# Performance work log

Hardware: AMD Instinct MI355X
Metric: run time of the kernel (lower is better)

## Reference

```python
import jax, jax.numpy as jnp
import numpy as np

B, N, C, F = 64, 64, 8, 256      # batch, neighbors per sample, in_channels, in_features
OC, OF = 8, 256                  # out_channels, out_features


def setup_inputs() -> dict:
    key = jax.random.key(0)
    k0, k1, k2, k3, k4 = jax.random.split(key, 5)
    x = jax.random.normal(k0, (B, C, F), dtype=jnp.float32)
    neighbor = jax.random.normal(k1, (B, N, C, F), dtype=jnp.float32)
    # att1/att2: nn.Linear(in_features, in_channels, bias=False) -> weight (C, F)
    W1 = jax.random.normal(k2, (C, F), dtype=jnp.float32) * (1.0 / np.sqrt(F))
    W2 = jax.random.normal(k3, (C, F), dtype=jnp.float32) * (1.0 / np.sqrt(F))
    # conv: nn.Conv1d(C, OC*OF, kernel_size=F, bias=False) -> weight (OC*OF, C, F)
    Wc = jax.random.normal(k4, (OC * OF, C, F), dtype=jnp.float32) * (1.0 / np.sqrt(C * F))
    return {"x": x, "neighbor": neighbor, "W1": W1, "W2": W2, "Wc": Wc}


def _sgnroot(a):
    return jnp.sign(a) * jnp.sqrt(jnp.clip(jnp.abs(a), 1e-8))


def _row_normalize(a):
    # torch: x / (x.abs().sum(1, keepdim=True) + 1e-7); dim 1 is the channel dim of (B,C,F,F)
    a = a / (jnp.abs(a).sum(axis=1, keepdims=True) + 1e-7)
    return jnp.where(jnp.isnan(a), 0.0, a)


def _feature_adjacency(x, neighbor, W1, W2):
    # w[b,n] = sum_{c,k} (x[b] @ W1^T)[c,k] * sum_{k,l} (neighbor[b,n] @ W2^T)[k,l]
    s1 = jnp.einsum('bcf,kf->b', x, W1)            # total sum of att1(x[b])
    s2 = jnp.einsum('bncf,kf->bn', neighbor, W2)   # total sum of att2(y[b,n])
    w = s1[:, None] * s2                            # (B, N)
    # fadj[b,c,a,d] = sum_n x[b,c,a] * neighbor[b,n,c,d] * w[b,n]
    fadj = jnp.einsum('bca,bncd,bn->bcad', x, neighbor, w)
    fadj = fadj + jnp.swapaxes(fadj, -2, -1)
    return _row_normalize(_sgnroot(fadj))


def _conv_transform(z, Wc, lead_shape):
    # Conv1d(C, OC*OF, kernel_size=F, bias=False) over (.., C, F) == full contraction
    out = jnp.einsum('...cf,ocf->...o', z, Wc)
    return out.reshape(*lead_shape, OC, OF)


def reference(x, neighbor, W1, W2, Wc):
    adj = _feature_adjacency(x, neighbor, W1, W2)              # (B,C,F,F)
    # transform(x, adj): (adj @ x.unsqueeze(-1)).squeeze(-1) then conv
    zx = jnp.einsum('bcad,bcd->bca', adj, x)                   # (B,C,F)
    x_out = _conv_transform(zx, Wc, (x.shape[0],))             # (B,OC,OF)
    # transform(neighbor[i], adj[i:i+1]) for each i -> adj broadcasts over N
    zn = jnp.einsum('bcad,bncd->bnca', adj, neighbor)          # (B,N,C,F)
    n_out = _conv_transform(zn, Wc, (x.shape[0], neighbor.shape[1]))  # (B,N,OC,OF)
    return x_out, n_out
```

## Files before the change

### kernel.cpp

```cpp
#include <hip/hip_runtime.h>
#include <hip/hip_bf16.h>
#include <math.h>

#define B_ 64
#define N_ 64
#define C_ 8
#define F_ 256
#define K_ 2048
#define NO_ 2048
#define M_TOT 4160

typedef __attribute__((ext_vector_type(8))) short bf16x8;
typedef __attribute__((ext_vector_type(4))) float f32x4;

__device__ __forceinline__ unsigned short bfbits(float f) {
    union { __hip_bfloat16 h; unsigned short u; } cv;
    cv.h = __float2bfloat16(f);
    return cv.u;
}

__global__ __launch_bounds__(256) void sums_wc_k(const float* __restrict__ x,
        const float* __restrict__ nb, const float* __restrict__ W1,
        const float* __restrict__ W2, const float* __restrict__ Wc,
        float* __restrict__ s1, float* __restrict__ s2,
        __hip_bfloat16* __restrict__ Bbuf) {
    int blk = blockIdx.x;
    int f = threadIdx.x;
    if (blk >= B_ * N_ + B_) {
        int i = (blk - (B_ * N_ + B_)) * 1024 + f * 4;
        float4 v = *(const float4*)(Wc + i);
        ushort4 u = { bfbits(v.x), bfbits(v.y), bfbits(v.z), bfbits(v.w) };
        *(ushort4*)(&Bbuf[i]) = u;
        return;
    }
    float val;
    if (blk < B_ * N_) {
        const float* base = nb + (size_t)blk * (C_ * F_);
        float wsum = 0.f;
        #pragma unroll
        for (int k = 0; k < C_; ++k) wsum += W2[k * F_ + f];
        float cs = 0.f;
        #pragma unroll
        for (int c = 0; c < C_; ++c) cs += base[c * F_ + f];
        val = cs * wsum;
    } else {
        int b = blk - B_ * N_;
        const float* base = x + (size_t)b * (C_ * F_);
        float wsum = 0.f;
        #pragma unroll
        for (int k = 0; k < C_; ++k) wsum += W1[k * F_ + f];
        float cs = 0.f;
        #pragma unroll
        for (int c = 0; c < C_; ++c) cs += base[c * F_ + f];
        val = cs * wsum;
    }
    #pragma unroll
    for (int off = 32; off > 0; off >>= 1) val += __shfl_down(val, off, 64);
    __shared__ float wred[4];
    int w = f >> 6;
    if ((f & 63) == 0) wred[w] = val;
    __syncthreads();
    if (f == 0) {
        float s = wred[0] + wred[1] + wred[2] + wred[3];
        if (blk < B_ * N_) s2[blk] = s;
        else s1[blk - B_ * N_] = s;
    }
}

__global__ __launch_bounds__(1024) void t_k(const float* __restrict__ nb,
        const float* __restrict__ s1, const float* __restrict__ s2,
        float* __restrict__ t) {
    int blk = blockIdx.x;
    int b = blk / C_, c = blk % C_;
    int tid = threadIdx.x;
    int q = tid >> 8, d = tid & 255;
    const float* p = nb + ((size_t)(b * N_) * C_ + c) * F_ + d;
    const float* s2p = s2 + b * N_;
    float acc = 0.f;
    #pragma unroll
    for (int j = 0; j < 16; ++j) {
        int n = q * 16 + j;
        acc += p[(size_t)n * C_ * F_] * s2p[n];
    }
    __shared__ float part[4][F_];
    part[q][d] = acc;
    __syncthreads();
    if (tid < 256) {
        float s = part[0][d] + part[1][d] + part[2][d] + part[3][d];
        t[(size_t)blk * F_ + d] = s * s1[b];
    }
}

__global__ __launch_bounds__(256) void denom_k(const float* __restrict__ x,
        const float* __restrict__ t, float* __restrict__ rdenom) {
    int blk = blockIdx.x;
    int b = blk >> 8, a = blk & 255;
    int d = threadIdx.x;
    float acc = 1e-7f;
    #pragma unroll
    for (int c = 0; c < C_; ++c) {
        size_t o = ((size_t)b * C_ + c) * F_;
        float xa = x[o + a], ta = t[o + a];
        float xd = x[o + d], td = t[o + d];
        float v = xa * td + xd * ta;
        float r = __builtin_amdgcn_sqrtf(fmaxf(fabsf(v), 1e-8f));
        acc += (v != 0.f) ? r : 0.f;
    }
    rdenom[(size_t)blk * F_ + d] = __builtin_amdgcn_rcpf(acc);
}

__device__ __forceinline__ float sgnroot_dev(float v) {
    float r = __builtin_amdgcn_sqrtf(fmaxf(fabsf(v), 1e-8f));
    return (v > 0.f) ? r : ((v < 0.f) ? -r : 0.f);
}

#define ZNX_PAD 264
__global__ __launch_bounds__(256, 2) void znx_k(const float* __restrict__ x,
        const float* __restrict__ t, const float* __restrict__ rdenom,
        const float* __restrict__ nb, __hip_bfloat16* __restrict__ Abuf) {
    int bc = blockIdx.x;
    int b = bc >> 3, c = bc & 7;
    int tid = threadIdx.x;
    int wave = tid >> 6, lane = tid & 63;
    __shared__ float xs[F_], ts[F_];
    __shared__ __hip_bfloat16 nbB[80 * ZNX_PAD];

    xs[tid] = x[(size_t)bc * F_ + tid];
    ts[tid] = t[(size_t)bc * F_ + tid];
    {
        int r = tid >> 2, cs0 = (tid & 3) * 64;
        const float* src = nb + (((size_t)(b * N_ + r)) * C_ + c) * F_ + cs0;
        __hip_bfloat16* dst = nbB + r * ZNX_PAD + cs0;
        #pragma unroll
        for (int j = 0; j < 64; j += 4) {
            float4 v = *(const float4*)(src + j);
            ushort4 u = { bfbits(v.x), bfbits(v.y), bfbits(v.z), bfbits(v.w) };
            *(ushort4*)(&dst[j]) = u;
        }
    }
    if (tid < 64) {
        float4 v = *(const float4*)(x + (size_t)bc * F_ + tid * 4);
        ushort4 u = { bfbits(v.x), bfbits(v.y), bfbits(v.z), bfbits(v.w) };
        *(ushort4*)(&nbB[64 * ZNX_PAD + tid * 4]) = u;
    }
    {
        __hip_bfloat16 z = __float2bfloat16(0.f);
        #pragma unroll
        for (int j = 0; j < 16; ++j) {
            int o = 65 * ZNX_PAD + tid * 16 + j;
            if (o < 80 * ZNX_PAD) nbB[o] = z;
        }
    }
    __syncthreads();

    const int aq = lane & 15;
    const int dq = lane >> 4;
    f32x4 acc[4][5] = {};
    #pragma unroll
    for (int atile = 0; atile < 4; ++atile) {
        int a = wave * 64 + atile * 16 + aq;
        float xa = xs[a], ta = ts[a];
        const float* drow = rdenom + ((size_t)b * F_ + a) * F_;
        #pragma unroll
        for (int kc = 0; kc < 8; ++kc) {
            int d0 = kc * 32 + dq * 8;
            float4 xv0 = *(const float4*)(xs + d0);
            float4 xv1 = *(const float4*)(xs + d0 + 4);
            float4 tv0 = *(const float4*)(ts + d0);
            float4 tv1 = *(const float4*)(ts + d0 + 4);
            float4 dn0 = *(const float4*)(drow + d0);
            float4 dn1 = *(const float4*)(drow + d0 + 4);
            float xv[8] = {xv0.x, xv0.y, xv0.z, xv0.w, xv1.x, xv1.y, xv1.z, xv1.w};
            float tv[8] = {tv0.x, tv0.y, tv0.z, tv0.w, tv1.x, tv1.y, tv1.z, tv1.w};
            float dn[8] = {dn0.x, dn0.y, dn0.z, dn0.w, dn1.x, dn1.y, dn1.z, dn1.w};
            union { bf16x8 v; __hip_bfloat16 h[8]; } bu;
            #pragma unroll
            for (int j = 0; j < 8; ++j) {
                float g = sgnroot_dev(xa * tv[j] + xv[j] * ta);
                bu.h[j] = __float2bfloat16(g * dn[j]);
            }
            #pragma unroll
            for (int mt = 0; mt < 5; ++mt) {
                bf16x8 af = *(const bf16x8*)(nbB + (mt * 16 + aq) * ZNX_PAD
                                             + kc * 32 + dq * 8);
                acc[atile][mt] = __builtin_amdgcn_mfma_f32_16x16x32_bf16(
                    af, bu.v, acc[atile][mt], 0, 0, 0);
            }
        }
    }

    __syncthreads();
    #pragma unroll
    for (int atile = 0; atile < 4; ++atile) {
        int a = wave * 64 + atile * 16 + aq;
        #pragma unroll
        for (int mt = 0; mt < 4; ++mt) {
            #pragma unroll
            for (int i = 0; i < 4; ++i) {
                int n = mt * 16 + dq * 4 + i;
                nbB[n * ZNX_PAD + a] = __float2bfloat16(acc[atile][mt][i]);
            }
        }
        if (dq == 0)
            nbB[64 * ZNX_PAD + a] = __float2bfloat16(acc[atile][4][0]);
    }
    __syncthreads();
    for (int it = 0; it < 17; ++it) {
        int q = it * 256 + tid;
        if (q < 4160) {
            int row = q >> 6;
            int off = (q & 63) * 4;
            ushort4 u = *(const ushort4*)(&nbB[row * ZNX_PAD + off]);
            int grow = (row < 64) ? (64 + b * N_ + row) : b;
            *(ushort4*)(&Abuf[(size_t)grow * K_ + c * F_ + off]) = u;
        }
    }
}

__global__ __launch_bounds__(256, 3) void gemm_bf16_k(
        const __hip_bfloat16* __restrict__ A,
        const __hip_bfloat16* __restrict__ Bm,
        float* __restrict__ Cm) {
    __shared__ char lds[49152] __attribute__((aligned(16)));
    const int t = threadIdx.x;
    const int wave = t >> 6;
    const int lane = t & 63;
    const int bidlin = blockIdx.y * 16 + blockIdx.x;
    const int bsw = (bidlin & 7) * 66 + (bidlin >> 3);
    const int col0 = (bsw & 15) * 128;
    const int row0 = (bsw >> 4) * 128;
    const int wrow0 = (wave & 1) * 64;
    const int wcol0 = (wave >> 1) * 64;
    const int aq = lane & 15;
    const int dq = lane >> 4;

    const int rA0 = t >> 2;
    const int kcs = ((t & 3) - ((t >> 3) & 3)) & 3;
    const int kc = kcs * 8;
    const int grA0 = min(row0 + rA0, M_TOT - 1);
    const int grA1 = min(row0 + rA0 + 64, M_TOT - 1);
    const int gcB0 = col0 + rA0;
    const int gcB1 = col0 + rA0 + 64;
    const size_t aoff0 = (size_t)grA0 * K_ + kc;
    const size_t aoff1 = (size_t)grA1 * K_ + kc;
    const size_t boff0 = (size_t)gcB0 * K_ + kc;
    const size_t boff1 = (size_t)gcB1 * K_ + kc;
    const int swz = ((dq + (aq >> 1)) & 3) * 16;
    const int ldsw = wave * 1024;

    f32x4 acc[4][4] = {};
    bf16x8 afr[2][4], bfr[2][4];

#define STAGE(BI, TK) do {                                                     \
    const int k0_ = (TK) * 32;                                                 \
    char* la_ = lds + (BI) * 16384 + ldsw;                                     \
    char* lb_ = la_ + 8192;                                                    \
    __builtin_amdgcn_global_load_lds(                                          \
        (const __attribute__((address_space(1))) void*)(A + aoff0 + k0_),      \
        (__attribute__((address_space(3))) void*)la_, 16, 0, 0);               \
    __builtin_amdgcn_global_load_lds(                                          \
        (const __attribute__((address_space(1))) void*)(A + aoff1 + k0_),      \
        (__attribute__((address_space(3))) void*)(la_ + 4096), 16, 0, 0);      \
    __builtin_amdgcn_global_load_lds(                                          \
        (const __attribute__((address_space(1))) void*)(Bm + boff0 + k0_),     \
        (__attribute__((address_space(3))) void*)lb_, 16, 0, 0);               \
    __builtin_amdgcn_global_load_lds(                                          \
        (const __attribute__((address_space(1))) void*)(Bm + boff1 + k0_),     \
        (__attribute__((address_space(3))) void*)(lb_ + 4096), 16, 0, 0);      \
} while (0)

#define DSREAD(BI, RI) do {                                                    \
    const char* la_ = lds + (BI) * 16384;                                      \
    const char* lb_ = la_ + 8192;                                              \
    _Pragma("unroll")                                                          \
    for (int rb = 0; rb < 4; ++rb)                                             \
        afr[RI][rb] = *(const bf16x8*)(la_ + (wrow0 + rb * 16 + aq) * 64 + swz);\
    _Pragma("unroll")                                                          \
    for (int cb = 0; cb < 4; ++cb)                                             \
        bfr[RI][cb] = *(const bf16x8*)(lb_ + (wcol0 + cb * 16 + aq) * 64 + swz);\
} while (0)

#define MFMAS(RI) do {                                                         \
    _Pragma("unroll")                                                          \
    for (int rb = 0; rb < 4; ++rb)                                             \
        _Pragma("unroll")                                                      \
        for (int cb = 0; cb < 4; ++cb)                                         \
            acc[rb][cb] = __builtin_amdgcn_mfma_f32_16x16x32_bf16(             \
                afr[RI][rb], bfr[RI][cb], acc[rb][cb], 0, 0, 0);               \
} while (0)

#define SYNC(NV) do {                                                          \
    asm volatile("s_waitcnt vmcnt(" #NV ") lgkmcnt(0)" ::: "memory");          \
    __builtin_amdgcn_sched_barrier(0);                                         \
    __builtin_amdgcn_s_barrier();                                              \
    __builtin_amdgcn_sched_barrier(0);                                         \
} while (0)

#define SLOT(BN, RN, BS, RC, TKS) do {                                         \
    SYNC(4);                                                                   \
    DSREAD(BN, RN);                                                            \
    STAGE(BS, TKS);                                                            \
    MFMAS(RC);                                                                 \
} while (0)

    STAGE(0, 0);
    STAGE(1, 1);
    STAGE(2, 2);
    asm volatile("s_waitcnt vmcnt(8)" ::: "memory");
    __builtin_amdgcn_sched_barrier(0);
    __builtin_amdgcn_s_barrier();
    __builtin_amdgcn_sched_barrier(0);
    DSREAD(0, 0);

    for (int s6 = 0; s6 < 60; s6 += 6) {
        SLOT(1, 1, 0, 0, s6 + 3);
        SLOT(2, 0, 1, 1, s6 + 4);
        SLOT(0, 1, 2, 0, s6 + 5);
        SLOT(1, 0, 0, 1, s6 + 6);
        SLOT(2, 1, 1, 0, s6 + 7);
        SLOT(0, 0, 2, 1, s6 + 8);
    }
    SLOT(1, 1, 0, 0, 63);
    SYNC(4);
    DSREAD(2, 0);
    MFMAS(1);
    SYNC(0);
    DSREAD(0, 1);
    MFMAS(0);
    MFMAS(1);

#undef STAGE
#undef DSREAD
#undef MFMAS
#undef SYNC
#undef SLOT

    #pragma unroll
    for (int rb = 0; rb < 4; ++rb) {
        int rowbase = row0 + wrow0 + rb * 16 + (lane >> 4) * 4;
        #pragma unroll
        for (int cb = 0; cb < 4; ++cb) {
            int col = col0 + wcol0 + cb * 16 + (lane & 15);
            #pragma unroll
            for (int i = 0; i < 4; ++i) {
                int row = rowbase + i;
                if (row < M_TOT)
                    Cm[(size_t)row * NO_ + col] = acc[rb][cb][i];
            }
        }
    }
}

extern "C" void kernel_launch(void* const* d_in, const int* in_sizes, int n_in,
                              void* d_out, int out_size, void* d_ws, size_t ws_size,
                              hipStream_t stream) {
    const float* x  = (const float*)d_in[0];
    const float* nb = (const float*)d_in[1];
    const float* W1 = (const float*)d_in[2];
    const float* W2 = (const float*)d_in[3];
    const float* Wc = (const float*)d_in[4];
    float* out = (float*)d_out;
    float* ws = (float*)d_ws;

    float* s1    = ws;
    float* s2    = ws + 64;
    float* t     = ws + 4160;
    float* rden  = ws + 135232;
    __hip_bfloat16* Abuf = (__hip_bfloat16*)(ws + 4329536);
    __hip_bfloat16* Bbuf = Abuf + (size_t)M_TOT * K_;

    hipLaunchKernelGGL(sums_wc_k, dim3(B_ * N_ + B_ + (K_ * NO_) / 1024),
                       dim3(256), 0, stream, x, nb, W1, W2, Wc, s1, s2, Bbuf);
    hipLaunchKernelGGL(t_k, dim3(B_ * C_), dim3(1024), 0, stream, nb, s1, s2, t);
    hipLaunchKernelGGL(denom_k, dim3(B_ * F_), dim3(256), 0, stream, x, t, rden);
    hipLaunchKernelGGL(znx_k, dim3(B_ * C_), dim3(256), 0, stream,
                       x, t, rden, nb, Abuf);
    hipLaunchKernelGGL(gemm_bf16_k, dim3(16, 33), dim3(256), 0, stream,
                       Abuf, Bbuf, out);
}
```

Baseline: 199.7 us.

## Switch GEMM to double-buffered K=64 tiles with XOR-swizzled LDS layout

Restructures the bf16 GEMM main loop from a triple-buffered K=32 pipeline into a double-buffered K=64 pipeline. Each stage now loads 128x64 tiles of A and B using an XOR swizzle over 16-byte chunks, and each wave issues two MFMAs per accumulator per tile. The goal is fewer barriers and waits per unit of K and better bank-conflict-free LDS reads. The cost is larger LDS use (64KB), which lowers the occupancy bound to 2 blocks, and a second barrier per slot before the buffer is overwritten.

```diff
diff --git a/kernel.cpp b/kernel.cpp
--- a/kernel.cpp
+++ b/kernel.cpp
@@ -217,11 +217,11 @@
     }
 }
 
-__global__ __launch_bounds__(256, 3) void gemm_bf16_k(
+__global__ __launch_bounds__(256, 2) void gemm_bf16_k(
         const __hip_bfloat16* __restrict__ A,
         const __hip_bfloat16* __restrict__ Bm,
         float* __restrict__ Cm) {
-    __shared__ char lds[49152] __attribute__((aligned(16)));
+    __shared__ char lds[65536] __attribute__((aligned(16)));
     const int t = threadIdx.x;
     const int wave = t >> 6;
     const int lane = t & 63;
@@ -234,105 +234,110 @@
     const int aq = lane & 15;
     const int dq = lane >> 4;
 
-    const int rA0 = t >> 2;
-    const int kcs = ((t & 3) - ((t >> 3) & 3)) & 3;
-    const int kc = kcs * 8;
-    const int grA0 = min(row0 + rA0, M_TOT - 1);
-    const int grA1 = min(row0 + rA0 + 64, M_TOT - 1);
-    const int gcB0 = col0 + rA0;
-    const int gcB1 = col0 + rA0 + 64;
-    const size_t aoff0 = (size_t)grA0 * K_ + kc;
-    const size_t aoff1 = (size_t)grA1 * K_ + kc;
-    const size_t boff0 = (size_t)gcB0 * K_ + kc;
-    const size_t boff1 = (size_t)gcB1 * K_ + kc;
-    const int swz = ((dq + (aq >> 1)) & 3) * 16;
-    const int ldsw = wave * 1024;
+    const int srow = t >> 3;
+    const int kce = (((t & 7) ^ (srow & 7)) * 8);
+    size_t aoffs[4], boffs[4];
+    #pragma unroll
+    for (int i = 0; i < 4; ++i) {
+        aoffs[i] = (size_t)min(row0 + srow + i * 32, M_TOT - 1) * K_ + kce;
+        boffs[i] = (size_t)(col0 + srow + i * 32) * K_ + kce;
+    }
+    const int ldst = t * 16;
+
+    const int sx = aq & 7;
+    int arow[4], brow[4];
+    #pragma unroll
+    for (int rb = 0; rb < 4; ++rb) {
+        arow[rb] = (wrow0 + rb * 16 + aq) * 128;
+        brow[rb] = (wcol0 + rb * 16 + aq) * 128;
+    }
+    int soff[2];
+    #pragma unroll
+    for (int kk = 0; kk < 2; ++kk) soff[kk] = ((kk * 4 + dq) ^ sx) * 16;
 
     f32x4 acc[4][4] = {};
-    bf16x8 afr[2][4], bfr[2][4];
+    bf16x8 af[4][2], bf[4][2];
 
 #define STAGE(BI, TK) do {                                                     \
-    const int k0_ = (TK) * 32;                                                 \
-    char* la_ = lds + (BI) * 16384 + ldsw;                                     \
-    char* lb_ = la_ + 8192;                                                    \
-    __builtin_amdgcn_global_load_lds(                                          \
-        (const __attribute__((address_space(1))) void*)(A + aoff0 + k0_),      \
-        (__attribute__((address_space(3))) void*)la_, 16, 0, 0);               \
-    __builtin_amdgcn_global_load_lds(                                          \
-        (const __attribute__((address_space(1))) void*)(A + aoff1 + k0_),      \
-        (__attribute__((address_space(3))) void*)(la_ + 4096), 16, 0, 0);      \
-    __builtin_amdgcn_global_load_lds(                                          \
-        (const __attribute__((address_space(1))) void*)(Bm + boff0 + k0_),     \
-        (__attribute__((address_space(3))) void*)lb_, 16, 0, 0);               \
-    __builtin_amdgcn_global_load_lds(                                          \
-        (const __attribute__((address_space(1))) void*)(Bm + boff1 + k0_),     \
-        (__attribute__((address_space(3))) void*)(lb_ + 4096), 16, 0, 0);      \
-} while (0)
-
-#define DSREAD(BI, RI) do {                                                    \
-    const char* la_ = lds + (BI) * 16384;                                      \
-    const char* lb_ = la_ + 8192;                                              \
-    _Pragma("unroll")                                                          \
-    for (int rb = 0; rb < 4; ++rb)                                             \
-        afr[RI][rb] = *(const bf16x8*)(la_ + (wrow0 + rb * 16 + aq) * 64 + swz);\
-    _Pragma("unroll")                                                          \
-    for (int cb = 0; cb < 4; ++cb)                                             \
-        bfr[RI][cb] = *(const bf16x8*)(lb_ + (wcol0 + cb * 16 + aq) * 64 + swz);\
-} while (0)
-
-#define MFMAS(RI) do {                                                         \
+    const int k0_ = (TK) * 64;                                                 \
+    char* la_ = lds + (BI) * 32768 + ldst;                                     \
+    char* lb_ = la_ + 16384;                                                   \
+    _Pragma("unroll")                                                          \
+    for (int i_ = 0; i_ < 4; ++i_)                                             \
+        __builtin_amdgcn_global_load_lds(                                      \
+            (const __attribute__((address_space(1))) void*)(A + aoffs[i_] + k0_),\
+            (__attribute__((address_space(3))) void*)(la_ + i_ * 4096), 16, 0, 0);\
+    _Pragma("unroll")                                                          \
+    for (int i_ = 0; i_ < 4; ++i_)                                             \
+        __builtin_amdgcn_global_load_lds(                                      \
+            (const __attribute__((address_space(1))) void*)(Bm + boffs[i_] + k0_),\
+            (__attribute__((address_space(3))) void*)(lb_ + i_ * 4096), 16, 0, 0);\
+} while (0)
+
+#define DSREAD(BI) do {                                                        \
+    const char* la_ = lds + (BI) * 32768;                                      \
+    const char* lb_ = la_ + 16384;                                             \
+    _Pragma("unroll")                                                          \
+    for (int rb = 0; rb < 4; ++rb) {                                           \
+        af[rb][0] = *(const bf16x8*)(la_ + arow[rb] + soff[0]);                \
+        af[rb][1] = *(const bf16x8*)(la_ + arow[rb] + soff[1]);                \
+    }                                                                          \
+    _Pragma("unroll")                                                          \
+    for (int cb = 0; cb < 4; ++cb) {                                           \
+        bf[cb][0] = *(const bf16x8*)(lb_ + brow[cb] + soff[0]);                \
+        bf[cb][1] = *(const bf16x8*)(lb_ + brow[cb] + soff[1]);                \
+    }                                                                          \
+} while (0)
+
+#define MFMAS() do {                                                           \
     _Pragma("unroll")                                                          \
     for (int rb = 0; rb < 4; ++rb)                                             \
         _Pragma("unroll")                                                      \
-        for (int cb = 0; cb < 4; ++cb)                                         \
+        for (int cb = 0; cb < 4; ++cb) {                                       \
             acc[rb][cb] = __builtin_amdgcn_mfma_f32_16x16x32_bf16(             \
-                afr[RI][rb], bfr[RI][cb], acc[rb][cb], 0, 0, 0);               \
-} while (0)
-
-#define SYNC(NV) do {                                                          \
-    asm volatile("s_waitcnt vmcnt(" #NV ") lgkmcnt(0)" ::: "memory");          \
+                af[rb][0], bf[cb][0], acc[rb][cb], 0, 0, 0);                   \
+            acc[rb][cb] = __builtin_amdgcn_mfma_f32_16x16x32_bf16(             \
+                af[rb][1], bf[cb][1], acc[rb][cb], 0, 0, 0);                   \
+        }                                                                      \
+} while (0)
+
+#define SYNCV(N) do {                                                          \
+    asm volatile("s_waitcnt vmcnt(" #N ")" ::: "memory");                      \
     __builtin_amdgcn_sched_barrier(0);                                         \
     __builtin_amdgcn_s_barrier();                                              \
     __builtin_amdgcn_sched_barrier(0);                                         \
 } while (0)
 
-#define SLOT(BN, RN, BS, RC, TKS) do {                                         \
-    SYNC(4);                                                                   \
-    DSREAD(BN, RN);                                                            \
-    STAGE(BS, TKS);                                                            \
-    MFMAS(RC);                                                                 \
+#define SLOT(BI, TKS) do {                                                     \
+    SYNCV(8);                                                                  \
+    DSREAD(BI);                                                                \
+    asm volatile("s_waitcnt lgkmcnt(0)" ::: "memory");                         \
+    __builtin_amdgcn_sched_barrier(0);                                         \
+    __builtin_amdgcn_s_barrier();                                              \
+    __builtin_amdgcn_sched_barrier(0);                                         \
+    STAGE(BI, TKS);                                                            \
+    __builtin_amdgcn_sched_barrier(0);                                         \
+    MFMAS();                                                                   \
 } while (0)
 
     STAGE(0, 0);
     STAGE(1, 1);
-    STAGE(2, 2);
-    asm volatile("s_waitcnt vmcnt(8)" ::: "memory");
-    __builtin_amdgcn_sched_barrier(0);
-    __builtin_amdgcn_s_barrier();
-    __builtin_amdgcn_sched_barrier(0);
-    DSREAD(0, 0);
-
-    for (int s6 = 0; s6 < 60; s6 += 6) {
-        SLOT(1, 1, 0, 0, s6 + 3);
-        SLOT(2, 0, 1, 1, s6 + 4);
-        SLOT(0, 1, 2, 0, s6 + 5);
-        SLOT(1, 0, 0, 1, s6 + 6);
-        SLOT(2, 1, 1, 0, s6 + 7);
-        SLOT(0, 0, 2, 1, s6 + 8);
-    }
-    SLOT(1, 1, 0, 0, 63);
-    SYNC(4);
-    DSREAD(2, 0);
-    MFMAS(1);
-    SYNC(0);
-    DSREAD(0, 1);
-    MFMAS(0);
-    MFMAS(1);
+
+    for (int tt = 0; tt < 30; tt += 2) {
+        SLOT(0, tt + 2);
+        SLOT(1, tt + 3);
+    }
+    SYNCV(8);
+    DSREAD(0);
+    MFMAS();
+    SYNCV(0);
+    DSREAD(1);
+    MFMAS();
 
 #undef STAGE
 #undef DSREAD
 #undef MFMAS
-#undef SYNC
+#undef SYNCV
 #undef SLOT
 
     #pragma unroll
```

New measurement: 196.1 us. No clear change (-1.8%).
